# Kernel optimization log

Hardware: AMD Instinct MI355X
Metric: run time of the kernel (lower is better)

## Reference

```python
import jax, jax.numpy as jnp
import numpy as np


def batch_pairwise_dist(x, y):
    # x: (B, Nx, 3), y: (B, Ny, 3) -> P: (B, Nx, Ny) squared euclidean dists
    xx = jnp.sum(x * x, axis=-1)                      # (B, Nx)
    yy = jnp.sum(y * y, axis=-1)                      # (B, Ny)
    zz = jnp.einsum('bnd,bmd->bnm', x, y)             # (B, Nx, Ny)
    return xx[:, :, None] + yy[:, None, :] - 2.0 * zz


def huber(x, c):
    return jnp.where(x < c, 0.5 * x * x, c * x - 0.5 * c * c)


def global_align_loss(preds, gts, c):
    # preds, gts: (B, N, 3) point sets; faithful to GlobalAlignLoss.forward
    P = batch_pairwise_dist(gts, preds)               # (B, Ngt, Npred)
    loss_1 = jnp.sum(huber(jnp.min(P, axis=1), c))
    loss_2 = jnp.sum(huber(jnp.min(P, axis=2), c))
    return loss_1 + loss_2


def setup_inputs() -> dict:
    key = jax.random.key(0)
    ks = jax.random.split(key, 8)
    B, KP, K, N = 4, 512, 32, 4096
    return {
        'src_keypoints': jax.random.normal(ks[0], (B, 3, KP), dtype=jnp.float32),
        'tgt_keypoints': jax.random.normal(ks[1], (B, 3, KP), dtype=jnp.float32),
        'rotation_ab': jax.random.normal(ks[2], (B, 3, 3), dtype=jnp.float32),
        'translation_ab': jax.random.normal(ks[3], (B, 3), dtype=jnp.float32),
        'src_keypoints_knn': jax.random.normal(ks[4], (B, 3, KP, K), dtype=jnp.float32),
        'tgt_keypoints_knn': jax.random.normal(ks[5], (B, 3, KP, K), dtype=jnp.float32),
        'k': K,
        'src_transformed': jax.random.normal(ks[6], (B, 3, N), dtype=jnp.float32),
        'tgt': jax.random.normal(ks[7], (B, 3, N), dtype=jnp.float32),
    }


def reference(src_keypoints, tgt_keypoints, rotation_ab, translation_ab,
              src_keypoints_knn, tgt_keypoints_knn, k, src_transformed, tgt):
    margin = 0.01  # loss_margin from init
    # Global alignment loss on full clouds (points last -> points first)
    gal = global_align_loss(jnp.transpose(src_transformed, (0, 2, 1)),
                            jnp.transpose(tgt, (0, 2, 1)), margin)
    # se3.transform: p' = R @ p + t, applied to keypoints (B, 3, KP)
    transformed_srckps = jnp.einsum('bij,bjn->bin', rotation_ab, src_keypoints) \
        + translation_ab[:, :, None]
    keypoints_loss = jnp.sum((transformed_srckps - tgt_keypoints) ** 2)
    knn_consensus_loss = jnp.sum((src_keypoints_knn - tgt_keypoints_knn) ** 2)
    neighborhood_consensus_loss = knn_consensus_loss / k + keypoints_loss
    return (neighborhood_consensus_loss, gal)
```

## Files before the change

### kernel.cpp

```cpp
#include <hip/hip_runtime.h>

#define NPTS 4096
#define NB   4
#define KP   512
#define HUBER_C 0.01f
#define HALF_PTS (NB * NPTS)
#define TOT_PTS  (2 * NB * NPTS)
#define OSTRIPE 64
#define QCHUNK  1024
#define NOC (NPTS / OSTRIPE)
#define NQC (NPTS / QCHUNK)
#define GAL_BLOCKS (2 * NB * NQC * NOC)

typedef float v2f __attribute__((ext_vector_type(2)));




__device__ inline void wave_reduce_add_to(float v, float* target) {
    #pragma unroll
    for (int off = 32; off; off >>= 1) v += __shfl_down(v, off, 64);
    if ((threadIdx.x & 63) == 0) atomicAdd(target, v);
}

__device__ inline float huber_f(float x) {
    return (x < HUBER_C) ? 0.5f * x * x
                         : fmaf(HUBER_C, x, -0.5f * HUBER_C * HUBER_C);
}

__device__ inline v2f splat2(float s) { v2f r; r.x = s; r.y = s; return r; }


__global__ __launch_bounds__(256) void init_kernel(
    uint4* __restrict__ minarr4, unsigned* __restrict__ ctrl)
{
    int i = blockIdx.x * 256 + threadIdx.x;
    minarr4[i] = make_uint4(0x7F800000u, 0x7F800000u, 0x7F800000u, 0x7F800000u);
    if (i == 0) ctrl[0] = 0u;
}

__global__ __launch_bounds__(256, 6) void main_kernel(
    const float* __restrict__ srcT, const float* __restrict__ tgtT,
    unsigned* __restrict__ minarr,
    const float* __restrict__ skp, const float* __restrict__ tkp,
    const float* __restrict__ R, const float* __restrict__ T,
    const float* __restrict__ aknn, const float* __restrict__ bknn,
    const int* __restrict__ kptr, float* __restrict__ acc,
    int knn_blocks, int knn_quads)
{
    __shared__ float4 olds[OSTRIPE];
    const int bid = blockIdx.x;
    const int tid = threadIdx.x;

    if (bid < GAL_BLOCKS) {
        const int oc  = bid & (NOC - 1);
        const int b   = (bid >> 6) & 3;
        const int dir = (bid >> 8) & 1;
        const int qc  = bid >> 9;
        const float* qb = (dir ? tgtT : srcT) + b * 3 * NPTS;
        const float* ob = (dir ? srcT : tgtT) + b * 3 * NPTS;

        if (tid < OSTRIPE) {
            int oi = oc * OSTRIPE + tid;
            float ox = ob[oi], oy = ob[NPTS + oi], oz = ob[2 * NPTS + oi];
            olds[tid] = make_float4(ox, oy, oz,
                                    fmaf(ox, ox, fmaf(oy, oy, oz * oz)));
        }

        v2f ax2[2], ay2[2], az2[2], mm2[2];
        float qw[4];
        #pragma unroll
        for (int p = 0; p < 2; ++p) {
            int ia = qc * QCHUNK + (2 * p) * 256 + tid;
            int ib = ia + 256;
            float Ax = qb[ia], Ay = qb[NPTS + ia], Az = qb[2 * NPTS + ia];
            float Bx = qb[ib], By = qb[NPTS + ib], Bz = qb[2 * NPTS + ib];
            ax2[p].x = -2.0f * Ax; ax2[p].y = -2.0f * Bx;
            ay2[p].x = -2.0f * Ay; ay2[p].y = -2.0f * By;
            az2[p].x = -2.0f * Az; az2[p].y = -2.0f * Bz;
            qw[2 * p]     = fmaf(Ax, Ax, fmaf(Ay, Ay, Az * Az));
            qw[2 * p + 1] = fmaf(Bx, Bx, fmaf(By, By, Bz * Bz));
            mm2[p].x = 3.0e38f; mm2[p].y = 3.0e38f;
        }
        __syncthreads();

        auto step2 = [&](const float4& u, const float4& v) {
            #pragma unroll
            for (int p = 0; p < 2; ++p) {
                v2f t0 = __builtin_elementwise_fma(splat2(u.x), ax2[p],
                         __builtin_elementwise_fma(splat2(u.y), ay2[p],
                         __builtin_elementwise_fma(splat2(u.z), az2[p], splat2(u.w))));
                v2f t1 = __builtin_elementwise_fma(splat2(v.x), ax2[p],
                         __builtin_elementwise_fma(splat2(v.y), ay2[p],
                         __builtin_elementwise_fma(splat2(v.z), az2[p], splat2(v.w))));
                mm2[p].x = fminf(mm2[p].x, fminf(t0.x, t1.x));
                mm2[p].y = fminf(mm2[p].y, fminf(t0.y, t1.y));
            }
        };

        #pragma unroll 4
        for (int j = 0; j < OSTRIPE; j += 4) {
            float4 o0 = olds[j], o1 = olds[j + 1];
            float4 o2 = olds[j + 2], o3 = olds[j + 3];
            step2(o0, o1);
            step2(o2, o3);
        }

        unsigned* marr = minarr + (dir * NB + b) * NPTS + qc * QCHUNK + tid;
        #pragma unroll
        for (int p = 0; p < 2; ++p) {
            float d0 = fmaxf(qw[2 * p]     + mm2[p].x, 0.0f);
            float d1 = fmaxf(qw[2 * p + 1] + mm2[p].y, 0.0f);
            atomicMin(&marr[(2 * p) * 256],     __float_as_uint(d0));
            atomicMin(&marr[(2 * p + 1) * 256], __float_as_uint(d1));
        }
    } else if (bid < GAL_BLOCKS + knn_blocks) {
        int i = (bid - GAL_BLOCKS) * 256 + tid;
        float sum = 0.0f;
        if (i < knn_quads) {
            float4 va = ((const float4*)aknn)[i];
            float4 vb = ((const float4*)bknn)[i];
            float dx = va.x - vb.x, dy = va.y - vb.y;
            float dz = va.z - vb.z, dw = va.w - vb.w;
            sum = fmaf(dx, dx, fmaf(dy, dy, fmaf(dz, dz, dw * dw)));
        }
        float scale = 1.0f / (float)(*kptr);
        wave_reduce_add_to(sum * scale, acc);
    } else {
        int i = (bid - GAL_BLOCKS - knn_blocks) * 256 + tid;
        int b = i >> 9;
        int n = i & (KP - 1);
        const float* r = R + b * 9;
        const float* t = T + b * 3;
        const float* s = skp + b * 3 * KP;
        const float* g = tkp + b * 3 * KP;
        float sx = s[n], sy = s[KP + n], sz = s[2 * KP + n];
        float sum = 0.0f;
        #pragma unroll
        for (int d = 0; d < 3; ++d) {
            float v = fmaf(r[d*3+0], sx, fmaf(r[d*3+1], sy, fmaf(r[d*3+2], sz, t[d])))
                      - g[d * KP + n];
            sum = fmaf(v, v, sum);
        }
        wave_reduce_add_to(sum, acc);
    }
}

__global__ __launch_bounds__(1024) void finalize_kernel(
    const unsigned* __restrict__ minarr, const float* __restrict__ acc,
    float* __restrict__ out)
{
    __shared__ float red[16];
    const int tid = threadIdx.x;
    const uint4* m4 = (const uint4*)minarr;
    float sum = 0.0f;
    #pragma unroll
    for (int r = 0; r < 8; ++r) {
        uint4 v = m4[r * 1024 + tid];
        sum += huber_f(__uint_as_float(v.x)) + huber_f(__uint_as_float(v.y))
             + huber_f(__uint_as_float(v.z)) + huber_f(__uint_as_float(v.w));
    }
    #pragma unroll
    for (int off = 32; off; off >>= 1) sum += __shfl_down(sum, off, 64);
    if ((tid & 63) == 0) red[tid >> 6] = sum;
    __syncthreads();
    if (tid == 0) {
        float s = 0.0f;
        #pragma unroll
        for (int i = 0; i < 16; ++i) s += red[i];
        out[1] = s;
        out[0] = *acc;
    }
}


__global__ void zero_out_kernel(float* __restrict__ out) {
    if (threadIdx.x < 2) out[threadIdx.x] = 0.0f;
}

__global__ __launch_bounds__(256) void gal_direct_kernel(
    const float* __restrict__ srcT, const float* __restrict__ tgtT,
    float* __restrict__ gal_out)
{
    const int dir = blockIdx.y >> 2;
    const int b   = blockIdx.y & 3;
    const float* qb = (dir ? tgtT : srcT) + b * 3 * NPTS;
    const float* ob = (dir ? srcT : tgtT) + b * 3 * NPTS;
    const int qi = blockIdx.x * 256 + threadIdx.x;
    const float qx = qb[qi], qy = qb[NPTS + qi], qz = qb[2 * NPTS + qi];
    float m = 3.0e38f;
    #pragma unroll 4
    for (int j = 0; j < NPTS; ++j) {
        float dx = qx - ob[j], dy = qy - ob[NPTS + j], dz = qz - ob[2 * NPTS + j];
        m = fminf(m, fmaf(dx, dx, fmaf(dy, dy, dz * dz)));
    }
    wave_reduce_add_to(huber_f(m), gal_out);
}

__global__ __launch_bounds__(256) void kp_kernel(
    const float* __restrict__ skp, const float* __restrict__ tkp,
    const float* __restrict__ R, const float* __restrict__ T,
    float* __restrict__ acc)
{
    int i = blockIdx.x * 256 + threadIdx.x;
    int b = i >> 9, n = i & (KP - 1);
    const float* r = R + b * 9;
    const float* t = T + b * 3;
    const float* s = skp + b * 3 * KP;
    const float* g = tkp + b * 3 * KP;
    float sx = s[n], sy = s[KP + n], sz = s[2 * KP + n];
    float sum = 0.0f;
    #pragma unroll
    for (int d = 0; d < 3; ++d) {
        float v = fmaf(r[d*3+0], sx, fmaf(r[d*3+1], sy, fmaf(r[d*3+2], sz, t[d])))
                  - g[d * KP + n];
        sum = fmaf(v, v, sum);
    }
    wave_reduce_add_to(sum, acc);
}

__global__ __launch_bounds__(256) void knn_kernel(
    const float* __restrict__ a, const float* __restrict__ b,
    const int* __restrict__ kptr, float* __restrict__ acc, int quads)
{
    int i = blockIdx.x * 256 + threadIdx.x;
    float sum = 0.0f;
    if (i < quads) {
        float4 va = ((const float4*)a)[i];
        float4 vb = ((const float4*)b)[i];
        float dx = va.x - vb.x, dy = va.y - vb.y;
        float dz = va.z - vb.z, dw = va.w - vb.w;
        sum = fmaf(dx, dx, fmaf(dy, dy, fmaf(dz, dz, dw * dw)));
    }
    float scale = 1.0f / (float)(*kptr);
    wave_reduce_add_to(sum * scale, acc);
}


extern "C" void kernel_launch(void* const* d_in, const int* in_sizes, int n_in,
                              void* d_out, int out_size, void* d_ws, size_t ws_size,
                              hipStream_t stream) {
    const float* skp  = (const float*)d_in[0];
    const float* tkp  = (const float*)d_in[1];
    const float* R    = (const float*)d_in[2];
    const float* T    = (const float*)d_in[3];
    const float* aknn = (const float*)d_in[4];
    const float* bknn = (const float*)d_in[5];
    const int*   kptr = (const int*)d_in[6];
    const float* srcT = (const float*)d_in[7];
    const float* tgtT = (const float*)d_in[8];
    float* out = (float*)d_out;

    const int knn_quads  = in_sizes[4] / 4;
    const int knn_blocks = (knn_quads + 255) / 256;
    const int kp_blocks  = (NB * KP + 255) / 256;

    const size_t min_bytes = (size_t)TOT_PTS * 4;
    const size_t ws_need   = min_bytes + 64;
    if (ws_size >= ws_need) {
        unsigned* minarr = (unsigned*)d_ws;
        unsigned* ctrl   = (unsigned*)((char*)d_ws + min_bytes);
        float*    acc    = (float*)&ctrl[0];
        init_kernel<<<TOT_PTS / 4 / 256, 256, 0, stream>>>((uint4*)minarr, ctrl);
        main_kernel<<<GAL_BLOCKS + knn_blocks + kp_blocks, 256, 0, stream>>>(
            srcT, tgtT, minarr, skp, tkp, R, T, aknn, bknn, kptr, acc,
            knn_blocks, knn_quads);
        finalize_kernel<<<1, 1024, 0, stream>>>(minarr, acc, out);
    } else {
        zero_out_kernel<<<1, 64, 0, stream>>>(out);
        gal_direct_kernel<<<dim3(NPTS / 256, 2 * NB), 256, 0, stream>>>(srcT, tgtT, out + 1);
        kp_kernel<<<kp_blocks, 256, 0, stream>>>(skp, tkp, R, T, out);
        knn_kernel<<<knn_blocks, 256, 0, stream>>>(aknn, bknn, kptr, out, knn_quads);
    }
}
```

Before: 91.74 us.

## Fuse finalize into main kernel via last-block counters and reorder block roles

Removes the separate finalize kernel. Each group of 64 GAL blocks that shares a query chunk counts its finished blocks with an atomic counter, and the last block applies Huber to that chunk's minima and adds the result to a global accumulator. A global done counter lets the last block of the whole grid write both outputs. The small knn and keypoint blocks are moved to the front of the grid. This saves one kernel launch and the serial single-block reduction, at the cost of extra atomics and fences at the end of every block.

Measured after the change: 155.3 us. 69.3% more time.

```diff
diff --git a/kernel.cpp b/kernel.cpp
--- a/kernel.cpp
+++ b/kernel.cpp
@@ -11,6 +11,8 @@
 #define NOC (NPTS / OSTRIPE)
 #define NQC (NPTS / QCHUNK)
 #define GAL_BLOCKS (2 * NB * NQC * NOC)
+#define NGRP (2 * NB * NQC)
+#define NCTRL 35
 
 typedef float v2f __attribute__((ext_vector_type(2)));
 
@@ -36,7 +38,7 @@
 {
     int i = blockIdx.x * 256 + threadIdx.x;
     minarr4[i] = make_uint4(0x7F800000u, 0x7F800000u, 0x7F800000u, 0x7F800000u);
-    if (i == 0) ctrl[0] = 0u;
+    if (blockIdx.x == 0 && threadIdx.x < NCTRL) ctrl[threadIdx.x] = 0u;
 }
 
 __global__ __launch_bounds__(256, 6) void main_kernel(
@@ -45,18 +47,28 @@
     const float* __restrict__ skp, const float* __restrict__ tkp,
     const float* __restrict__ R, const float* __restrict__ T,
     const float* __restrict__ aknn, const float* __restrict__ bknn,
-    const int* __restrict__ kptr, float* __restrict__ acc,
-    int knn_blocks, int knn_quads)
+    const int* __restrict__ kptr, unsigned* __restrict__ ctrl,
+    float* __restrict__ out,
+    int knn_blocks, int knn_quads, int total_blocks)
 {
     __shared__ float4 olds[OSTRIPE];
+    float* accp = (float*)&ctrl[0];
+    float* galp = (float*)&ctrl[1];
+    unsigned* donep = &ctrl[2];
+    unsigned* grpcnt = &ctrl[3];
+
     const int bid = blockIdx.x;
     const int tid = threadIdx.x;
-
-    if (bid < GAL_BLOCKS) {
-        const int oc  = bid & (NOC - 1);
-        const int b   = (bid >> 6) & 3;
-        const int dir = (bid >> 8) & 1;
-        const int qc  = bid >> 9;
+    const int kp_blocks = (NB * KP) / 256;
+    const int pre = knn_blocks + kp_blocks;
+
+    if (bid >= pre) {
+        const int gb  = bid - pre;
+        const int oc  = gb & (NOC - 1);
+        const int b   = (gb >> 6) & 3;
+        const int dir = (gb >> 8) & 1;
+        const int qc  = gb >> 9;
+        const int grp = gb >> 6;
         const float* qb = (dir ? tgtT : srcT) + b * 3 * NPTS;
         const float* ob = (dir ? srcT : tgtT) + b * 3 * NPTS;
 
@@ -114,8 +126,29 @@
             atomicMin(&marr[(2 * p) * 256],     __float_as_uint(d0));
             atomicMin(&marr[(2 * p + 1) * 256], __float_as_uint(d1));
         }
-    } else if (bid < GAL_BLOCKS + knn_blocks) {
-        int i = (bid - GAL_BLOCKS) * 256 + tid;
+
+        __syncthreads();
+        __shared__ unsigned role;
+        if (tid == 0) {
+            __threadfence();
+            role = (atomicAdd(&grpcnt[grp], 1u) == (unsigned)(NOC - 1));
+        }
+        __syncthreads();
+        if (role) {
+            __threadfence();
+            const unsigned* gm = minarr + (dir * NB + b) * NPTS + qc * QCHUNK;
+            float s = 0.0f;
+            #pragma unroll
+            for (int k2 = 0; k2 < 4; ++k2) {
+                unsigned mv = __hip_atomic_load(&gm[tid + 256 * k2],
+                                                __ATOMIC_RELAXED,
+                                                __HIP_MEMORY_SCOPE_AGENT);
+                s += huber_f(__uint_as_float(mv));
+            }
+            wave_reduce_add_to(s, galp);
+        }
+    } else if (bid < knn_blocks) {
+        int i = bid * 256 + tid;
         float sum = 0.0f;
         if (i < knn_quads) {
             float4 va = ((const float4*)aknn)[i];
@@ -125,9 +158,9 @@
             sum = fmaf(dx, dx, fmaf(dy, dy, fmaf(dz, dz, dw * dw)));
         }
         float scale = 1.0f / (float)(*kptr);
-        wave_reduce_add_to(sum * scale, acc);
+        wave_reduce_add_to(sum * scale, accp);
     } else {
-        int i = (bid - GAL_BLOCKS - knn_blocks) * 256 + tid;
+        int i = (bid - knn_blocks) * 256 + tid;
         int b = i >> 9;
         int n = i & (KP - 1);
         const float* r = R + b * 9;
@@ -142,34 +175,24 @@
                       - g[d * KP + n];
             sum = fmaf(v, v, sum);
         }
-        wave_reduce_add_to(sum, acc);
-    }
-}
-
-__global__ __launch_bounds__(1024) void finalize_kernel(
-    const unsigned* __restrict__ minarr, const float* __restrict__ acc,
-    float* __restrict__ out)
-{
-    __shared__ float red[16];
-    const int tid = threadIdx.x;
-    const uint4* m4 = (const uint4*)minarr;
-    float sum = 0.0f;
-    #pragma unroll
-    for (int r = 0; r < 8; ++r) {
-        uint4 v = m4[r * 1024 + tid];
-        sum += huber_f(__uint_as_float(v.x)) + huber_f(__uint_as_float(v.y))
-             + huber_f(__uint_as_float(v.z)) + huber_f(__uint_as_float(v.w));
-    }
-    #pragma unroll
-    for (int off = 32; off; off >>= 1) sum += __shfl_down(sum, off, 64);
-    if ((tid & 63) == 0) red[tid >> 6] = sum;
+        wave_reduce_add_to(sum, accp);
+    }
+
     __syncthreads();
+    __shared__ unsigned lastflag;
     if (tid == 0) {
-        float s = 0.0f;
-        #pragma unroll
-        for (int i = 0; i < 16; ++i) s += red[i];
-        out[1] = s;
-        out[0] = *acc;
+        __threadfence();
+        lastflag = (atomicAdd(donep, 1u) == (unsigned)(total_blocks - 1));
+    }
+    __syncthreads();
+    if (lastflag && tid == 0) {
+        __threadfence();
+        unsigned a = __hip_atomic_load(&ctrl[0], __ATOMIC_RELAXED,
+                                       __HIP_MEMORY_SCOPE_AGENT);
+        unsigned g2 = __hip_atomic_load(&ctrl[1], __ATOMIC_RELAXED,
+                                        __HIP_MEMORY_SCOPE_AGENT);
+        out[0] = __uint_as_float(a);
+        out[1] = __uint_as_float(g2);
     }
 }
 
@@ -256,16 +279,15 @@
     const int kp_blocks  = (NB * KP + 255) / 256;
 
     const size_t min_bytes = (size_t)TOT_PTS * 4;
-    const size_t ws_need   = min_bytes + 64;
+    const size_t ws_need   = min_bytes + NCTRL * 4;
     if (ws_size >= ws_need) {
         unsigned* minarr = (unsigned*)d_ws;
         unsigned* ctrl   = (unsigned*)((char*)d_ws + min_bytes);
-        float*    acc    = (float*)&ctrl[0];
+        const int total  = knn_blocks + kp_blocks + GAL_BLOCKS;
         init_kernel<<<TOT_PTS / 4 / 256, 256, 0, stream>>>((uint4*)minarr, ctrl);
-        main_kernel<<<GAL_BLOCKS + knn_blocks + kp_blocks, 256, 0, stream>>>(
-            srcT, tgtT, minarr, skp, tkp, R, T, aknn, bknn, kptr, acc,
-            knn_blocks, knn_quads);
-        finalize_kernel<<<1, 1024, 0, stream>>>(minarr, acc, out);
+        main_kernel<<<total, 256, 0, stream>>>(
+            srcT, tgtT, minarr, skp, tkp, R, T, aknn, bknn, kptr, ctrl, out,
+            knn_blocks, knn_quads, total);
     } else {
         zero_out_kernel<<<1, 64, 0, stream>>>(out);
         gal_direct_kernel<<<dim3(NPTS / 256, 2 * NB), 256, 0, stream>>>(srcT, tgtT, out + 1);
```
